# Performance work log

Measured on AMD Instinct MI355X. Metric: run time of the kernel, lower is better.

Reference implementation:

```python
import jax, jax.numpy as jnp
import numpy as np

N_U, N_V = 8192, 8192
IN_U, IN_V = 64, 64
OUT_U, OUT_V = 64, 64
RATING = 5


def setup_inputs() -> dict:
    key = jax.random.key(0)
    k1, k2, k3, k4, k5 = jax.random.split(key, 5)
    adj = jax.random.randint(k1, (N_U, N_V), 0, 6, dtype=jnp.int32)  # ratings 0..5, 0 = no edge
    u_feature = jax.random.normal(k2, (N_U, IN_U), dtype=jnp.float32)
    v_feature = jax.random.normal(k3, (N_V, IN_V), dtype=jnp.float32)
    weight_u = 0.02 * jax.random.normal(k4, (RATING, IN_V, OUT_U), dtype=jnp.float32)
    weight_v = 0.02 * jax.random.normal(k5, (RATING, IN_U, OUT_V), dtype=jnp.float32)
    return {"adj": adj, "u_feature": u_feature, "v_feature": v_feature,
            "weight_u": weight_u, "weight_v": weight_v}


def reference(adj, u_feature, v_feature, weight_u, weight_v):
    rating = weight_u.shape[0]
    dt = u_feature.dtype
    # Per-rating binary masks M_r: [R, n_u, n_v]
    ratings = jnp.arange(1, rating + 1, dtype=adj.dtype)
    masks = (adj[None, :, :] == ratings[:, None, None]).astype(dt)
    # Degree normalization (reciprocal of nonzero counts; inf -> 0)
    deg_u = jnp.sum(adj > 0, axis=1).astype(dt)  # [n_u]
    deg_v = jnp.sum(adj > 0, axis=0).astype(dt)  # [n_v]
    d_u = jnp.where(deg_u > 0, 1.0 / deg_u, 0.0)
    d_v = jnp.where(deg_v > 0, 1.0 / deg_v, 0.0)
    # Aggregate neighbor features per rating, project, sum over ratings.
    agg_u = jnp.einsum('ruv,vf->ruf', masks, v_feature)      # [R, n_u, in_v]
    out_u = jnp.einsum('ruf,rfo->uo', agg_u, weight_u)        # [n_u, out_u]
    out_u = d_u[:, None] * out_u
    agg_v = jnp.einsum('ruv,uf->rvf', masks, u_feature)      # [R, n_v, in_u]
    out_v = jnp.einsum('rvf,rfo->vo', agg_v, weight_v)        # [n_v, out_v]
    out_v = d_v[:, None] * out_v
    return (jax.nn.relu(out_u), jax.nn.relu(out_v))
```

## Files before the change

### kernel.cpp

```cpp
#include <hip/hip_runtime.h>

#define N_U 8192
#define N_V 8192
#define DIM 64
#define NR 5

typedef __attribute__((ext_vector_type(8))) short short8;
typedef __attribute__((ext_vector_type(4))) float f32x4;

__device__ inline unsigned short f2bf(float x) {
    unsigned u = __float_as_uint(x);
    return (unsigned short)((u + 0x7FFFu + ((u >> 16) & 1u)) >> 16);
}

__device__ inline size_t pfrag_idx(int r, int k, int o) {
    int ktile = k >> 5;
    int lane  = ((k >> 2) & 3) * 16 + (o & 15);
    int j     = ((k >> 4) & 1) * 4 + (k & 3);
    int n     = o >> 4;
    return ((((size_t)r * (N_V / 32) + ktile) * 4 + n) * 64 + lane) * 8 + j;
}

__global__ __launch_bounds__(256) void precompute_P(
    const float* __restrict__ u_feat, const float* __restrict__ v_feat,
    const float* __restrict__ w_u, const float* __restrict__ w_v,
    unsigned short* __restrict__ p_u, unsigned short* __restrict__ p_v)
{
    int wid  = (blockIdx.x * blockDim.x + threadIdx.x) >> 6;
    int lane = threadIdx.x & 63;
    const int tasks = 2 * NR * (N_V / 32);
    if (wid >= tasks) return;
    int dir  = wid / (NR * (N_V / 32));
    int rem  = wid % (NR * (N_V / 32));
    int r    = rem / (N_V / 32);
    int v0   = (rem % (N_V / 32)) * 32;

    const float* feat = dir ? u_feat : v_feat;
    const float* w    = dir ? w_v : w_u;
    unsigned short* dst = dir ? p_v : p_u;

    float wreg[DIM];
#pragma unroll
    for (int f = 0; f < DIM; ++f) wreg[f] = w[(r * DIM + f) * DIM + lane];

    for (int v = v0; v < v0 + 32; ++v) {
        float x = feat[(size_t)v * DIM + lane];
        float acc = 0.f;
#pragma unroll
        for (int f = 0; f < DIM; ++f) acc += __shfl(x, f) * wreg[f];
        dst[pfrag_idx(r, v, lane)] = f2bf(acc);
    }
}

template <int TRANS>
__global__ __launch_bounds__(512) void gemm_masked(
    const int* __restrict__ adj, const unsigned short* __restrict__ pfrag,
    float* __restrict__ outp, unsigned int* __restrict__ deg)
{
    __shared__ unsigned char tile[256 * 72];
    __shared__ unsigned int cnt[256];

    const int tid  = threadIdx.x;
    const int lane = tid & 63;
    const int wv   = tid >> 6;
    const int b0   = blockIdx.x * 256;
    const int k0b  = blockIdx.y * 512;

    if (tid < 256) cnt[tid] = 0;
    __syncthreads();

    f32x4 acc[2][4];
#pragma unroll
    for (int m = 0; m < 2; ++m)
#pragma unroll
        for (int n = 0; n < 4; ++n) acc[m][n] = (f32x4){0.f, 0.f, 0.f, 0.f};

    for (int kk = 0; kk < 512; kk += 64) {
        const int k0 = k0b + kk;
        if (TRANS == 0) {
#pragma unroll
            for (int it = 0; it < 8; ++it) {
                int idx4 = it * 512 + tid;
                int row  = idx4 >> 4;
                int c4   = (idx4 & 15) * 4;
                int4 a = *(const int4*)(adj + (size_t)(b0 + row) * N_V + (k0 + c4));
                unsigned packed = (a.x & 0xFF) | ((a.y & 0xFF) << 8) |
                                  ((a.z & 0xFF) << 16) | ((a.w & 0xFF) << 24);
                *(unsigned*)&tile[row * 72 + c4] = packed;
                unsigned c = (a.x != 0) + (a.y != 0) + (a.z != 0) + (a.w != 0);
                if (c) atomicAdd(&cnt[row], c);
            }
        } else {
#pragma unroll
            for (int it = 0; it < 2; ++it) {
                int bi = it * 512 + tid;
                int u4 = (bi >> 6) * 4;
                int v4 = (bi & 63) * 4;
                int4 d0 = *(const int4*)(adj + (size_t)(k0 + u4 + 0) * N_V + (b0 + v4));
                int4 d1 = *(const int4*)(adj + (size_t)(k0 + u4 + 1) * N_V + (b0 + v4));
                int4 d2 = *(const int4*)(adj + (size_t)(k0 + u4 + 2) * N_V + (b0 + v4));
                int4 d3 = *(const int4*)(adj + (size_t)(k0 + u4 + 3) * N_V + (b0 + v4));
                const int* p0 = (const int*)&d0; const int* p1 = (const int*)&d1;
                const int* p2 = (const int*)&d2; const int* p3 = (const int*)&d3;
#pragma unroll
                for (int c = 0; c < 4; ++c) {
                    int x0 = p0[c], x1 = p1[c], x2 = p2[c], x3 = p3[c];
                    unsigned packed = (x0 & 0xFF) | ((x1 & 0xFF) << 8) |
                                      ((x2 & 0xFF) << 16) | ((x3 & 0xFF) << 24);
                    *(unsigned*)&tile[(v4 + c) * 72 + u4] = packed;
                    unsigned cc = (x0 != 0) + (x1 != 0) + (x2 != 0) + (x3 != 0);
                    if (cc) atomicAdd(&cnt[v4 + c], cc);
                }
            }
        }
        __syncthreads();

#pragma unroll
        for (int k32 = 0; k32 < 64; k32 += 32) {
            const int ktile = (k0 + k32) >> 5;
            short8 amask[2][NR];
#pragma unroll
            for (int m = 0; m < 2; ++m) {
                int row  = wv * 32 + m * 16 + (lane & 15);
                int boff = row * 72 + k32 + ((lane >> 4) << 2);
                unsigned d0 = *(const unsigned*)&tile[boff];
                unsigned d1 = *(const unsigned*)&tile[boff + 16];
#pragma unroll
                for (int rr = 0; rr < NR; ++rr) {
                    short8 msk;
#pragma unroll
                    for (int j = 0; j < 4; ++j)
                        msk[j] = (short)((((d0 >> (8 * j)) & 0xFFu) == (unsigned)(rr + 1)) ? 0x3F80 : 0);
#pragma unroll
                    for (int j = 0; j < 4; ++j)
                        msk[4 + j] = (short)((((d1 >> (8 * j)) & 0xFFu) == (unsigned)(rr + 1)) ? 0x3F80 : 0);
                    amask[m][rr] = msk;
                }
            }
#pragma unroll
            for (int n = 0; n < 4; ++n) {
#pragma unroll
                for (int rr = 0; rr < NR; ++rr) {
                    const unsigned short* bp =
                        pfrag + ((((size_t)rr * (N_V / 32) + ktile) * 4 + n) * 64 + lane) * 8;
                    short8 bfrag = *(const short8*)bp;
                    acc[0][n] = __builtin_amdgcn_mfma_f32_16x16x32_bf16(amask[0][rr], bfrag, acc[0][n], 0, 0, 0);
                    acc[1][n] = __builtin_amdgcn_mfma_f32_16x16x32_bf16(amask[1][rr], bfrag, acc[1][n], 0, 0, 0);
                }
            }
        }
        __syncthreads();
    }

#pragma unroll
    for (int m = 0; m < 2; ++m) {
        int rbase = b0 + wv * 32 + m * 16 + ((lane >> 4) << 2);
#pragma unroll
        for (int n = 0; n < 4; ++n) {
#pragma unroll
            for (int q = 0; q < 4; ++q) {
                atomicAdd(&outp[(size_t)(rbase + q) * DIM + n * 16 + (lane & 15)], acc[m][n][q]);
            }
        }
    }
    if (tid < 256) atomicAdd(&deg[b0 + tid], cnt[tid]);
}

__global__ __launch_bounds__(256) void finalize_k(
    float* __restrict__ outp, const unsigned int* __restrict__ deg_u,
    const unsigned int* __restrict__ deg_v)
{
    int idx = blockIdx.x * blockDim.x + threadIdx.x;
    const int total = 2 * N_U * DIM;
    for (; idx < total; idx += gridDim.x * blockDim.x) {
        int row = idx >> 6;
        unsigned d = (row < N_U) ? deg_u[row] : deg_v[row - N_U];
        float s = d ? (1.f / (float)d) : 0.f;
        float v = outp[idx] * s;
        outp[idx] = v > 0.f ? v : 0.f;
    }
}

extern "C" void kernel_launch(void* const* d_in, const int* in_sizes, int n_in,
                              void* d_out, int out_size, void* d_ws, size_t ws_size,
                              hipStream_t stream)
{
    const int*   adj = (const int*)d_in[0];
    const float* uf  = (const float*)d_in[1];
    const float* vf  = (const float*)d_in[2];
    const float* wu  = (const float*)d_in[3];
    const float* wv  = (const float*)d_in[4];
    float* outp = (float*)d_out;

    unsigned char* ws = (unsigned char*)d_ws;
    const size_t P_BYTES = (size_t)NR * (N_V / 32) * 4 * 64 * 8 * 2;
    unsigned short* p_u  = (unsigned short*)ws;
    unsigned short* p_v  = (unsigned short*)(ws + P_BYTES);
    unsigned int*   deg_u = (unsigned int*)(ws + 2 * P_BYTES);
    unsigned int*   deg_v = (unsigned int*)(ws + 2 * P_BYTES + N_U * sizeof(unsigned int));

    hipMemsetAsync(d_out, 0, (size_t)2 * N_U * DIM * sizeof(float), stream);
    hipMemsetAsync(ws + 2 * P_BYTES, 0, (N_U + N_V) * sizeof(unsigned int), stream);

    precompute_P<<<640, 256, 0, stream>>>(uf, vf, wu, wv, p_u, p_v);

    dim3 grid(32, 16);
    gemm_masked<0><<<grid, 512, 0, stream>>>(adj, p_u, outp, deg_u);
    gemm_masked<1><<<grid, 512, 0, stream>>>(adj, p_v, outp + (size_t)N_U * DIM, deg_v);

    finalize_k<<<2048, 256, 0, stream>>>(outp, deg_u, deg_v);
}
```

Baseline: 335.0 us.

## Double-buffer adj and P tiles with async LDS loads in masked GEMM

Restructures the masked GEMM main loop into a two-stage software pipeline. P fragments are staged into shared memory with global_load_lds, and the next step's adjacency tile is prefetched into registers while MFMAs run on the current buffer. The adjacency tile shrinks to 32-wide K steps with a swizzled LDS layout to cut bank conflicts. Degree counting now uses per-thread packed register counters reduced once at the end instead of shared-memory atomics. It adds register pressure (launch bounds asks for 4 blocks) and a more complex synchronisation pattern.

```diff
diff --git a/kernel.cpp b/kernel.cpp
--- a/kernel.cpp
+++ b/kernel.cpp
@@ -4,6 +4,9 @@
 #define N_V 8192
 #define DIM 64
 #define NR 5
+#define BM 256
+#define NSTEP 16
+#define KS 32
 
 typedef __attribute__((ext_vector_type(8))) short short8;
 typedef __attribute__((ext_vector_type(4))) float f32x4;
@@ -11,6 +14,12 @@
 __device__ inline unsigned short f2bf(float x) {
     unsigned u = __float_as_uint(x);
     return (unsigned short)((u + 0x7FFFu + ((u >> 16) & 1u)) >> 16);
+}
+
+__device__ __forceinline__ void gload_lds16(const void* g, void* l) {
+    __builtin_amdgcn_global_load_lds(
+        (const __attribute__((address_space(1))) void*)g,
+        (__attribute__((address_space(3))) void*)l, 16, 0, 0);
 }
 
 __device__ inline size_t pfrag_idx(int r, int k, int o) {
@@ -53,102 +62,137 @@
 }
 
 template <int TRANS>
-__global__ __launch_bounds__(512) void gemm_masked(
+__global__ __launch_bounds__(512, 4) void gemm_masked(
     const int* __restrict__ adj, const unsigned short* __restrict__ pfrag,
     float* __restrict__ outp, unsigned int* __restrict__ deg)
 {
-    __shared__ unsigned char tile[256 * 72];
-    __shared__ unsigned int cnt[256];
+    __shared__ unsigned char  bufA[2][BM][40];
+    __shared__ unsigned short bufB[2][NR][4][64][8];
 
     const int tid  = threadIdx.x;
     const int lane = tid & 63;
     const int wv   = tid >> 6;
-    const int b0   = blockIdx.x * 256;
-    const int k0b  = blockIdx.y * 512;
-
-    if (tid < 256) cnt[tid] = 0;
+    const int b0   = blockIdx.x * BM;
+    const int kt0  = blockIdx.y * NSTEP;
+
+    f32x4 acc[2][4];
+#pragma unroll
+    for (int m = 0; m < 2; ++m)
+#pragma unroll
+        for (int n = 0; n < 4; ++n) acc[m][n] = (f32x4){0.f, 0.f, 0.f, 0.f};
+
+    unsigned cnt_pack = 0;
+    int4 pre[4];
+
+    auto issueB = [&](int s) {
+        const int p = s & 1;
+        const int kt = kt0 + s;
+        for (int c = wv; c < 20; c += 8) {
+            int rr = c >> 2, n = c & 3;
+            const unsigned short* src =
+                pfrag + ((((size_t)rr * (N_V / 32) + kt) * 4 + n) << 9) + lane * 8;
+            gload_lds16(src, (void*)&bufB[p][rr][n][0][0]);
+        }
+    };
+    auto loadAdj = [&](int s) {
+        const int kbase = (kt0 + s) * KS;
+        if (TRANS == 0) {
+#pragma unroll
+            for (int it = 0; it < 4; ++it) {
+                int idx4 = it * 512 + tid;
+                int row  = idx4 >> 3;
+                int c4   = (idx4 & 7) * 4;
+                pre[it] = *(const int4*)(adj + (size_t)(b0 + row) * N_V + (kbase + c4));
+            }
+        } else {
+            int u4 = (tid >> 6) * 4;
+            int v4 = (tid & 63) * 4;
+#pragma unroll
+            for (int c = 0; c < 4; ++c)
+                pre[c] = *(const int4*)(adj + (size_t)(kbase + u4 + c) * N_V + (b0 + v4));
+        }
+    };
+    auto packWrite = [&](int s) {
+        const int p = s & 1;
+        if (TRANS == 0) {
+#pragma unroll
+            for (int it = 0; it < 4; ++it) {
+                int idx4 = it * 512 + tid;
+                int row  = idx4 >> 3;
+                int c4   = (idx4 & 7) * 4;
+                int4 a = pre[it];
+                unsigned pk = (a.x & 0xFF) | ((a.y & 0xFF) << 8) |
+                              ((a.z & 0xFF) << 16) | ((a.w & 0xFF) << 24);
+                int w = ((c4 >> 2) + (row >> 4)) & 7;
+                *(unsigned*)&bufA[p][row][w * 4] = pk;
+                unsigned c = (a.x != 0) + (a.y != 0) + (a.z != 0) + (a.w != 0);
+                cnt_pack += c << (8 * it);
+            }
+        } else {
+            int u4 = (tid >> 6) * 4;
+            int v4 = (tid & 63) * 4;
+            const int* q0 = (const int*)&pre[0];
+            const int* q1 = (const int*)&pre[1];
+            const int* q2 = (const int*)&pre[2];
+            const int* q3 = (const int*)&pre[3];
+#pragma unroll
+            for (int cc = 0; cc < 4; ++cc) {
+                int x0 = q0[cc], x1 = q1[cc], x2 = q2[cc], x3 = q3[cc];
+                unsigned pk = (x0 & 0xFF) | ((x1 & 0xFF) << 8) |
+                              ((x2 & 0xFF) << 16) | ((x3 & 0xFF) << 24);
+                int row = v4 + cc;
+                int w = ((u4 >> 2) + (row >> 4)) & 7;
+                *(unsigned*)&bufA[p][row][w * 4] = pk;
+                unsigned c = (x0 != 0) + (x1 != 0) + (x2 != 0) + (x3 != 0);
+                cnt_pack += c << (8 * cc);
+            }
+        }
+    };
+    auto compute = [&](int s) {
+        const int p = s & 1;
+        unsigned d[2][2];
+#pragma unroll
+        for (int m = 0; m < 2; ++m) {
+            int row = wv * 32 + m * 16 + (lane & 15);
+            int sw  = (row >> 4) & 7;
+            int lg  = lane >> 4;
+            d[m][0] = *(const unsigned*)&bufA[p][row][4 * ((lg + sw) & 7)];
+            d[m][1] = *(const unsigned*)&bufA[p][row][4 * ((lg + 4 + sw) & 7)];
+        }
+        unsigned bx[2][8];
+#pragma unroll
+        for (int m = 0; m < 2; ++m)
+#pragma unroll
+            for (int j = 0; j < 4; ++j) {
+                bx[m][j]     = (d[m][0] >> (8 * j)) & 0xFFu;
+                bx[m][4 + j] = (d[m][1] >> (8 * j)) & 0xFFu;
+            }
+#pragma unroll
+        for (int rr = 0; rr < NR; ++rr) {
+            short8 am[2];
+#pragma unroll
+            for (int m = 0; m < 2; ++m)
+#pragma unroll
+                for (int j = 0; j < 8; ++j)
+                    am[m][j] = (short)(bx[m][j] == (unsigned)(rr + 1) ? 0x3F80 : 0);
+#pragma unroll
+            for (int n = 0; n < 4; ++n) {
+                short8 bf = *(const short8*)&bufB[p][rr][n][lane][0];
+                acc[0][n] = __builtin_amdgcn_mfma_f32_16x16x32_bf16(am[0], bf, acc[0][n], 0, 0, 0);
+                acc[1][n] = __builtin_amdgcn_mfma_f32_16x16x32_bf16(am[1], bf, acc[1][n], 0, 0, 0);
+            }
+        }
+    };
+
+    issueB(0);
+    loadAdj(0);
+    packWrite(0);
     __syncthreads();
 
-    f32x4 acc[2][4];
-#pragma unroll
-    for (int m = 0; m < 2; ++m)
-#pragma unroll
-        for (int n = 0; n < 4; ++n) acc[m][n] = (f32x4){0.f, 0.f, 0.f, 0.f};
-
-    for (int kk = 0; kk < 512; kk += 64) {
-        const int k0 = k0b + kk;
-        if (TRANS == 0) {
-#pragma unroll
-            for (int it = 0; it < 8; ++it) {
-                int idx4 = it * 512 + tid;
-                int row  = idx4 >> 4;
-                int c4   = (idx4 & 15) * 4;
-                int4 a = *(const int4*)(adj + (size_t)(b0 + row) * N_V + (k0 + c4));
-                unsigned packed = (a.x & 0xFF) | ((a.y & 0xFF) << 8) |
-                                  ((a.z & 0xFF) << 16) | ((a.w & 0xFF) << 24);
-                *(unsigned*)&tile[row * 72 + c4] = packed;
-                unsigned c = (a.x != 0) + (a.y != 0) + (a.z != 0) + (a.w != 0);
-                if (c) atomicAdd(&cnt[row], c);
-            }
-        } else {
-#pragma unroll
-            for (int it = 0; it < 2; ++it) {
-                int bi = it * 512 + tid;
-                int u4 = (bi >> 6) * 4;
-                int v4 = (bi & 63) * 4;
-                int4 d0 = *(const int4*)(adj + (size_t)(k0 + u4 + 0) * N_V + (b0 + v4));
-                int4 d1 = *(const int4*)(adj + (size_t)(k0 + u4 + 1) * N_V + (b0 + v4));
-                int4 d2 = *(const int4*)(adj + (size_t)(k0 + u4 + 2) * N_V + (b0 + v4));
-                int4 d3 = *(const int4*)(adj + (size_t)(k0 + u4 + 3) * N_V + (b0 + v4));
-                const int* p0 = (const int*)&d0; const int* p1 = (const int*)&d1;
-                const int* p2 = (const int*)&d2; const int* p3 = (const int*)&d3;
-#pragma unroll
-                for (int c = 0; c < 4; ++c) {
-                    int x0 = p0[c], x1 = p1[c], x2 = p2[c], x3 = p3[c];
-                    unsigned packed = (x0 & 0xFF) | ((x1 & 0xFF) << 8) |
-                                      ((x2 & 0xFF) << 16) | ((x3 & 0xFF) << 24);
-                    *(unsigned*)&tile[(v4 + c) * 72 + u4] = packed;
-                    unsigned cc = (x0 != 0) + (x1 != 0) + (x2 != 0) + (x3 != 0);
-                    if (cc) atomicAdd(&cnt[v4 + c], cc);
-                }
-            }
-        }
-        __syncthreads();
-
-#pragma unroll
-        for (int k32 = 0; k32 < 64; k32 += 32) {
-            const int ktile = (k0 + k32) >> 5;
-            short8 amask[2][NR];
-#pragma unroll
-            for (int m = 0; m < 2; ++m) {
-                int row  = wv * 32 + m * 16 + (lane & 15);
-                int boff = row * 72 + k32 + ((lane >> 4) << 2);
-                unsigned d0 = *(const unsigned*)&tile[boff];
-                unsigned d1 = *(const unsigned*)&tile[boff + 16];
-#pragma unroll
-                for (int rr = 0; rr < NR; ++rr) {
-                    short8 msk;
-#pragma unroll
-                    for (int j = 0; j < 4; ++j)
-                        msk[j] = (short)((((d0 >> (8 * j)) & 0xFFu) == (unsigned)(rr + 1)) ? 0x3F80 : 0);
-#pragma unroll
-                    for (int j = 0; j < 4; ++j)
-                        msk[4 + j] = (short)((((d1 >> (8 * j)) & 0xFFu) == (unsigned)(rr + 1)) ? 0x3F80 : 0);
-                    amask[m][rr] = msk;
-                }
-            }
-#pragma unroll
-            for (int n = 0; n < 4; ++n) {
-#pragma unroll
-                for (int rr = 0; rr < NR; ++rr) {
-                    const unsigned short* bp =
-                        pfrag + ((((size_t)rr * (N_V / 32) + ktile) * 4 + n) * 64 + lane) * 8;
-                    short8 bfrag = *(const short8*)bp;
-                    acc[0][n] = __builtin_amdgcn_mfma_f32_16x16x32_bf16(amask[0][rr], bfrag, acc[0][n], 0, 0, 0);
-                    acc[1][n] = __builtin_amdgcn_mfma_f32_16x16x32_bf16(amask[1][rr], bfrag, acc[1][n], 0, 0, 0);
-                }
-            }
-        }
+    for (int s = 0; s < NSTEP; ++s) {
+        if (s + 1 < NSTEP) { issueB(s + 1); loadAdj(s + 1); }
+        compute(s);
+        if (s + 1 < NSTEP) packWrite(s + 1);
         __syncthreads();
     }
 
@@ -156,14 +200,29 @@
     for (int m = 0; m < 2; ++m) {
         int rbase = b0 + wv * 32 + m * 16 + ((lane >> 4) << 2);
 #pragma unroll
-        for (int n = 0; n < 4; ++n) {
-#pragma unroll
-            for (int q = 0; q < 4; ++q) {
+        for (int n = 0; n < 4; ++n)
+#pragma unroll
+            for (int q = 0; q < 4; ++q)
                 atomicAdd(&outp[(size_t)(rbase + q) * DIM + n * 16 + (lane & 15)], acc[m][n][q]);
-            }
-        }
-    }
-    if (tid < 256) atomicAdd(&deg[b0 + tid], cnt[tid]);
+    }
+
+    __syncthreads();
+    unsigned* sc = (unsigned*)&bufA[0][0][0];
+    sc[tid] = cnt_pack;
+    __syncthreads();
+    if (tid < BM) {
+        unsigned tot = 0;
+        if (TRANS == 0) {
+            int it = tid >> 6, srow = tid & 63;
+#pragma unroll
+            for (int j = 0; j < 8; ++j) tot += (sc[srow * 8 + j] >> (8 * it)) & 0xFFu;
+        } else {
+            int sv = tid >> 2, cc = tid & 3;
+#pragma unroll
+            for (int j = 0; j < 8; ++j) tot += (sc[sv + 64 * j] >> (8 * cc)) & 0xFFu;
+        }
+        atomicAdd(&deg[b0 + tid], tot);
+    }
 }
 
 __global__ __launch_bounds__(256) void finalize_k(
@@ -194,8 +253,8 @@
 
     unsigned char* ws = (unsigned char*)d_ws;
     const size_t P_BYTES = (size_t)NR * (N_V / 32) * 4 * 64 * 8 * 2;
-    unsigned short* p_u  = (unsigned short*)ws;
-    unsigned short* p_v  = (unsigned short*)(ws + P_BYTES);
+    unsigned short* p_u   = (unsigned short*)ws;
+    unsigned short* p_v   = (unsigned short*)(ws + P_BYTES);
     unsigned int*   deg_u = (unsigned int*)(ws + 2 * P_BYTES);
     unsigned int*   deg_v = (unsigned int*)(ws + 2 * P_BYTES + N_U * sizeof(unsigned int));
 
@@ -204,7 +263,7 @@
 
     precompute_P<<<640, 256, 0, stream>>>(uf, vf, wu, wv, p_u, p_v);
 
-    dim3 grid(32, 16);
+    dim3 grid(N_U / BM, 16);
     gemm_masked<0><<<grid, 512, 0, stream>>>(adj, p_u, outp, deg_u);
     gemm_masked<1><<<grid, 512, 0, stream>>>(adj, p_v, outp + (size_t)N_U * DIM, deg_v);
 
```

Result: slower. 454.8 us (+35.8%).

## Stage full adjacency tile as 4-bit nibbles in LDS with prefetched loads

Applied to the files above, without the earlier changes.

Each block now loads its entire 256x512 adjacency slab into shared memory in one phase, packed as 4-bit ratings in an XOR-swizzled layout, with register double-buffered global loads. Degree counting uses wave ballots and popcount, or per-thread packed byte counters, in place of shared atomics. The compute loop then runs with no barriers, and the B-fragment layout is changed so each lane's eight k values are contiguous. This removes per-chunk syncs and LDS atomics at the cost of larger shared memory use and higher register pressure.

```diff
diff --git a/kernel.cpp b/kernel.cpp
--- a/kernel.cpp
+++ b/kernel.cpp
@@ -4,6 +4,9 @@
 #define N_V 8192
 #define DIM 64
 #define NR 5
+#define BM 256
+#define BK 512
+#define NSTEP 16
 
 typedef __attribute__((ext_vector_type(8))) short short8;
 typedef __attribute__((ext_vector_type(4))) float f32x4;
@@ -15,8 +18,9 @@
 
 __device__ inline size_t pfrag_idx(int r, int k, int o) {
     int ktile = k >> 5;
-    int lane  = ((k >> 2) & 3) * 16 + (o & 15);
-    int j     = ((k >> 4) & 1) * 4 + (k & 3);
+    int g     = (k >> 3) & 3;
+    int j     = k & 7;
+    int lane  = g * 16 + (o & 15);
     int n     = o >> 4;
     return ((((size_t)r * (N_V / 32) + ktile) * 4 + n) * 64 + lane) * 8 + j;
 }
@@ -53,20 +57,84 @@
 }
 
 template <int TRANS>
-__global__ __launch_bounds__(512) void gemm_masked(
+__global__ __launch_bounds__(512, 4) void gemm_masked(
     const int* __restrict__ adj, const unsigned short* __restrict__ pfrag,
     float* __restrict__ outp, unsigned int* __restrict__ deg)
 {
-    __shared__ unsigned char tile[256 * 72];
-    __shared__ unsigned int cnt[256];
+    __shared__ unsigned char tile[BM][256];
+    __shared__ unsigned int  cnt[BM];
 
     const int tid  = threadIdx.x;
     const int lane = tid & 63;
     const int wv   = tid >> 6;
-    const int b0   = blockIdx.x * 256;
-    const int k0b  = blockIdx.y * 512;
-
-    if (tid < 256) cnt[tid] = 0;
+    const int b0   = blockIdx.x * BM;
+    const int k0   = blockIdx.y * BK;
+
+    unsigned cpack = 0;
+
+    if (TRANS == 0) {
+        int4 pre[4], nxt[4];
+        const int sub = tid & 31;
+        auto issue = [&](int rnd, int4* dst) {
+            int row = rnd * 16 + (tid >> 5);
+            const int* base = adj + (size_t)(b0 + row) * N_V + k0 + sub * 4;
+#pragma unroll
+            for (int it = 0; it < 4; ++it) dst[it] = *(const int4*)(base + it * 128);
+        };
+        issue(0, pre);
+        for (int rnd = 0; rnd < 16; ++rnd) {
+            if (rnd + 1 < 16) issue(rnd + 1, nxt);
+            int row = rnd * 16 + (tid >> 5);
+            unsigned lo = 0, hi = 0;
+#pragma unroll
+            for (int it = 0; it < 4; ++it) {
+                int4 a = pre[it];
+                unsigned long long bx = __ballot(a.x != 0), by = __ballot(a.y != 0);
+                unsigned long long bz = __ballot(a.z != 0), bw = __ballot(a.w != 0);
+                lo += __popcll(bx & 0xFFFFFFFFull) + __popcll(by & 0xFFFFFFFFull) +
+                      __popcll(bz & 0xFFFFFFFFull) + __popcll(bw & 0xFFFFFFFFull);
+                hi += __popcll(bx >> 32) + __popcll(by >> 32) +
+                      __popcll(bz >> 32) + __popcll(bw >> 32);
+                unsigned pk = (unsigned)a.x | ((unsigned)a.y << 4) |
+                              ((unsigned)a.z << 8) | ((unsigned)a.w << 12);
+                int d  = it * 16 + (sub >> 1);
+                int dp = d ^ (row & 31);
+                *(unsigned short*)&tile[row][dp * 4 + (sub & 1) * 2] = (unsigned short)pk;
+            }
+            if ((tid & 31) == 0) cnt[row] = (lane & 32) ? hi : lo;
+#pragma unroll
+            for (int it = 0; it < 4; ++it) pre[it] = nxt[it];
+        }
+    } else {
+        const int v4 = (tid & 63) * 4;
+        int4 pre[4], nxt[4];
+        auto issue = [&](int rnd, int4* dst) {
+            int u0 = rnd * 32 + (tid >> 6) * 4;
+#pragma unroll
+            for (int c = 0; c < 4; ++c)
+                dst[c] = *(const int4*)(adj + (size_t)(k0 + u0 + c) * N_V + b0 + v4);
+        };
+        issue(0, pre);
+        for (int rnd = 0; rnd < 16; ++rnd) {
+            if (rnd + 1 < 16) issue(rnd + 1, nxt);
+            const int* q0 = (const int*)&pre[0]; const int* q1 = (const int*)&pre[1];
+            const int* q2 = (const int*)&pre[2]; const int* q3 = (const int*)&pre[3];
+            int d    = rnd * 4 + ((tid >> 6) >> 1);
+            int half = (tid >> 6) & 1;
+#pragma unroll
+            for (int cc = 0; cc < 4; ++cc) {
+                int x0 = q0[cc], x1 = q1[cc], x2 = q2[cc], x3 = q3[cc];
+                unsigned pk = (unsigned)x0 | ((unsigned)x1 << 4) |
+                              ((unsigned)x2 << 8) | ((unsigned)x3 << 12);
+                int row = v4 + cc;
+                int dp  = d ^ (row & 31);
+                *(unsigned short*)&tile[row][dp * 4 + half * 2] = (unsigned short)pk;
+                cpack += (unsigned)((x0 != 0) + (x1 != 0) + (x2 != 0) + (x3 != 0)) << (8 * cc);
+            }
+#pragma unroll
+            for (int c = 0; c < 4; ++c) pre[c] = nxt[c];
+        }
+    }
     __syncthreads();
 
     f32x4 acc[2][4];
@@ -75,95 +143,64 @@
 #pragma unroll
         for (int n = 0; n < 4; ++n) acc[m][n] = (f32x4){0.f, 0.f, 0.f, 0.f};
 
-    for (int kk = 0; kk < 512; kk += 64) {
-        const int k0 = k0b + kk;
-        if (TRANS == 0) {
-#pragma unroll
-            for (int it = 0; it < 8; ++it) {
-                int idx4 = it * 512 + tid;
-                int row  = idx4 >> 4;
-                int c4   = (idx4 & 15) * 4;
-                int4 a = *(const int4*)(adj + (size_t)(b0 + row) * N_V + (k0 + c4));
-                unsigned packed = (a.x & 0xFF) | ((a.y & 0xFF) << 8) |
-                                  ((a.z & 0xFF) << 16) | ((a.w & 0xFF) << 24);
-                *(unsigned*)&tile[row * 72 + c4] = packed;
-                unsigned c = (a.x != 0) + (a.y != 0) + (a.z != 0) + (a.w != 0);
-                if (c) atomicAdd(&cnt[row], c);
+    const int mrow = wv * 32;
+    for (int s = 0; s < NSTEP; ++s) {
+        unsigned nib[2];
+#pragma unroll
+        for (int m = 0; m < 2; ++m) {
+            int row = mrow + m * 16 + (lane & 15);
+            int d   = s * 4 + (lane >> 4);
+            nib[m] = *(const unsigned*)&tile[row][((d ^ (row & 31)) << 2)];
+        }
+        const int ktg = (k0 >> 5) + s;
+#pragma unroll
+        for (int r = 0; r < NR; ++r) {
+            short8 bf[4];
+#pragma unroll
+            for (int n = 0; n < 4; ++n)
+                bf[n] = *(const short8*)(pfrag +
+                         ((((size_t)r * (N_V / 32) + ktg) * 4 + n) * 64 + lane) * 8);
+            short8 am[2];
+#pragma unroll
+            for (int m = 0; m < 2; ++m)
+#pragma unroll
+                for (int j = 0; j < 8; ++j) {
+                    unsigned nb = (nib[m] >> (4 * j)) & 0xFu;
+                    am[m][j] = (short)(nb == (unsigned)(r + 1) ? 0x3F80 : 0);
+                }
+#pragma unroll
+            for (int n = 0; n < 4; ++n) {
+                acc[0][n] = __builtin_amdgcn_mfma_f32_16x16x32_bf16(am[0], bf[n], acc[0][n], 0, 0, 0);
+                acc[1][n] = __builtin_amdgcn_mfma_f32_16x16x32_bf16(am[1], bf[n], acc[1][n], 0, 0, 0);
             }
-        } else {
-#pragma unroll
-            for (int it = 0; it < 2; ++it) {
-                int bi = it * 512 + tid;
-                int u4 = (bi >> 6) * 4;
-                int v4 = (bi & 63) * 4;
-                int4 d0 = *(const int4*)(adj + (size_t)(k0 + u4 + 0) * N_V + (b0 + v4));
-                int4 d1 = *(const int4*)(adj + (size_t)(k0 + u4 + 1) * N_V + (b0 + v4));
-                int4 d2 = *(const int4*)(adj + (size_t)(k0 + u4 + 2) * N_V + (b0 + v4));
-                int4 d3 = *(const int4*)(adj + (size_t)(k0 + u4 + 3) * N_V + (b0 + v4));
-                const int* p0 = (const int*)&d0; const int* p1 = (const int*)&d1;
-                const int* p2 = (const int*)&d2; const int* p3 = (const int*)&d3;
-#pragma unroll
-                for (int c = 0; c < 4; ++c) {
-                    int x0 = p0[c], x1 = p1[c], x2 = p2[c], x3 = p3[c];
-                    unsigned packed = (x0 & 0xFF) | ((x1 & 0xFF) << 8) |
-                                      ((x2 & 0xFF) << 16) | ((x3 & 0xFF) << 24);
-                    *(unsigned*)&tile[(v4 + c) * 72 + u4] = packed;
-                    unsigned cc = (x0 != 0) + (x1 != 0) + (x2 != 0) + (x3 != 0);
-                    if (cc) atomicAdd(&cnt[v4 + c], cc);
-                }
-            }
-        }
+        }
+    }
+
+#pragma unroll
+    for (int m = 0; m < 2; ++m) {
+        int rbase = b0 + mrow + m * 16 + ((lane >> 4) << 2);
+#pragma unroll
+        for (int n = 0; n < 4; ++n)
+#pragma unroll
+            for (int q = 0; q < 4; ++q)
+                atomicAdd(&outp[(size_t)(rbase + q) * DIM + n * 16 + (lane & 15)], acc[m][n][q]);
+    }
+
+    if (TRANS == 0) {
+        if (tid < BM) atomicAdd(&deg[b0 + tid], cnt[tid]);
+    } else {
         __syncthreads();
-
-#pragma unroll
-        for (int k32 = 0; k32 < 64; k32 += 32) {
-            const int ktile = (k0 + k32) >> 5;
-            short8 amask[2][NR];
-#pragma unroll
-            for (int m = 0; m < 2; ++m) {
-                int row  = wv * 32 + m * 16 + (lane & 15);
-                int boff = row * 72 + k32 + ((lane >> 4) << 2);
-                unsigned d0 = *(const unsigned*)&tile[boff];
-                unsigned d1 = *(const unsigned*)&tile[boff + 16];
-#pragma unroll
-                for (int rr = 0; rr < NR; ++rr) {
-                    short8 msk;
-#pragma unroll
-                    for (int j = 0; j < 4; ++j)
-                        msk[j] = (short)((((d0 >> (8 * j)) & 0xFFu) == (unsigned)(rr + 1)) ? 0x3F80 : 0);
-#pragma unroll
-                    for (int j = 0; j < 4; ++j)
-                        msk[4 + j] = (short)((((d1 >> (8 * j)) & 0xFFu) == (unsigned)(rr + 1)) ? 0x3F80 : 0);
-                    amask[m][rr] = msk;
-                }
-            }
-#pragma unroll
-            for (int n = 0; n < 4; ++n) {
-#pragma unroll
-                for (int rr = 0; rr < NR; ++rr) {
-                    const unsigned short* bp =
-                        pfrag + ((((size_t)rr * (N_V / 32) + ktile) * 4 + n) * 64 + lane) * 8;
-                    short8 bfrag = *(const short8*)bp;
-                    acc[0][n] = __builtin_amdgcn_mfma_f32_16x16x32_bf16(amask[0][rr], bfrag, acc[0][n], 0, 0, 0);
-                    acc[1][n] = __builtin_amdgcn_mfma_f32_16x16x32_bf16(amask[1][rr], bfrag, acc[1][n], 0, 0, 0);
-                }
-            }
-        }
+        unsigned* sc = (unsigned*)&tile[0][0];
+        sc[tid] = cpack;
         __syncthreads();
-    }
-
-#pragma unroll
-    for (int m = 0; m < 2; ++m) {
-        int rbase = b0 + wv * 32 + m * 16 + ((lane >> 4) << 2);
-#pragma unroll
-        for (int n = 0; n < 4; ++n) {
-#pragma unroll
-            for (int q = 0; q < 4; ++q) {
-                atomicAdd(&outp[(size_t)(rbase + q) * DIM + n * 16 + (lane & 15)], acc[m][n][q]);
-            }
-        }
-    }
-    if (tid < 256) atomicAdd(&deg[b0 + tid], cnt[tid]);
+        if (tid < BM) {
+            unsigned tot = 0;
+            int base = tid >> 2, byte = tid & 3;
+#pragma unroll
+            for (int j = 0; j < 8; ++j) tot += (sc[j * 64 + base] >> (8 * byte)) & 0xFFu;
+            atomicAdd(&deg[b0 + tid], tot);
+        }
+    }
 }
 
 __global__ __launch_bounds__(256) void finalize_k(
@@ -194,8 +231,8 @@
 
     unsigned char* ws = (unsigned char*)d_ws;
     const size_t P_BYTES = (size_t)NR * (N_V / 32) * 4 * 64 * 8 * 2;
-    unsigned short* p_u  = (unsigned short*)ws;
-    unsigned short* p_v  = (unsigned short*)(ws + P_BYTES);
+    unsigned short* p_u   = (unsigned short*)ws;
+    unsigned short* p_v   = (unsigned short*)(ws + P_BYTES);
     unsigned int*   deg_u = (unsigned int*)(ws + 2 * P_BYTES);
     unsigned int*   deg_v = (unsigned int*)(ws + 2 * P_BYTES + N_U * sizeof(unsigned int));
 
@@ -204,7 +241,7 @@
 
     precompute_P<<<640, 256, 0, stream>>>(uf, vf, wu, wv, p_u, p_v);
 
-    dim3 grid(32, 16);
+    dim3 grid(N_U / BM, N_V / BK);
     gemm_masked<0><<<grid, 512, 0, stream>>>(adj, p_u, outp, deg_u);
     gemm_masked<1><<<grid, 512, 0, stream>>>(adj, p_v, outp + (size_t)N_U * DIM, deg_v);
 
```

After: 286.0 us. -14.6%, faster.

## Give each block full-K rows, drop LDS staging, atomics, memsets and finalize kernel

Applied to the files above, without the earlier changes.

Each 512-thread block now owns 16 output rows and walks the whole K dimension, with its 8 waves striding over k-tiles. Waves load adjacency values straight into registers in the MFMA A-fragment layout, so the LDS byte tile is gone, and they count degrees in registers. A tree reduction through shared memory combines partial sums, then wave 0 applies the degree normalisation and ReLU and writes the output directly. This removes the global atomics, both memsets and the separate finalize kernel. In exchange, the transposed direction now does strided 4-byte scalar loads, only 512 blocks run per direction, and the P fragments are no longer reused across 32-row tiles.

```diff
diff --git a/kernel.cpp b/kernel.cpp
--- a/kernel.cpp
+++ b/kernel.cpp
@@ -1,7 +1,6 @@
 #include <hip/hip_runtime.h>
 
-#define N_U 8192
-#define N_V 8192
+#define NN 8192
 #define DIM 64
 #define NR 5
 
@@ -13,12 +12,13 @@
     return (unsigned short)((u + 0x7FFFu + ((u >> 16) & 1u)) >> 16);
 }
 
-__device__ inline size_t pfrag_idx(int r, int k, int o) {
+__device__ inline int pfrag_idx(int r, int k, int o) {
     int ktile = k >> 5;
-    int lane  = ((k >> 2) & 3) * 16 + (o & 15);
-    int j     = ((k >> 4) & 1) * 4 + (k & 3);
+    int g     = (k >> 3) & 3;
+    int j     = k & 7;
+    int lane  = g * 16 + (o & 15);
     int n     = o >> 4;
-    return ((((size_t)r * (N_V / 32) + ktile) * 4 + n) * 64 + lane) * 8 + j;
+    return ((r * 256 + ktile) * 4 + n) * 512 + lane * 8 + j;
 }
 
 __global__ __launch_bounds__(256) void precompute_P(
@@ -28,12 +28,12 @@
 {
     int wid  = (blockIdx.x * blockDim.x + threadIdx.x) >> 6;
     int lane = threadIdx.x & 63;
-    const int tasks = 2 * NR * (N_V / 32);
+    const int tasks = 2 * NR * (NN / 32);
     if (wid >= tasks) return;
-    int dir  = wid / (NR * (N_V / 32));
-    int rem  = wid % (NR * (N_V / 32));
-    int r    = rem / (N_V / 32);
-    int v0   = (rem % (N_V / 32)) * 32;
+    int dir  = wid / (NR * (NN / 32));
+    int rem  = wid % (NR * (NN / 32));
+    int r    = rem / (NN / 32);
+    int v0   = (rem % (NN / 32)) * 32;
 
     const float* feat = dir ? u_feat : v_feat;
     const float* w    = dir ? w_v : w_u;
@@ -52,132 +52,118 @@
     }
 }
 
-template <int TRANS>
-__global__ __launch_bounds__(512) void gemm_masked(
+template <int DIR>
+__global__ __launch_bounds__(512, 4) void gemm_dir(
     const int* __restrict__ adj, const unsigned short* __restrict__ pfrag,
-    float* __restrict__ outp, unsigned int* __restrict__ deg)
+    float* __restrict__ outp)
 {
-    __shared__ unsigned char tile[256 * 72];
-    __shared__ unsigned int cnt[256];
+    __shared__ float redf[4][16][66];
+    __shared__ int   redd[8][16];
 
     const int tid  = threadIdx.x;
     const int lane = tid & 63;
     const int wv   = tid >> 6;
-    const int b0   = blockIdx.x * 256;
-    const int k0b  = blockIdx.y * 512;
+    const int row  = lane & 15;
+    const int g    = lane >> 4;
+    const int b0   = blockIdx.x * 16;
 
-    if (tid < 256) cnt[tid] = 0;
-    __syncthreads();
+    f32x4 acc[4];
+#pragma unroll
+    for (int n = 0; n < 4; ++n) acc[n] = (f32x4){0.f, 0.f, 0.f, 0.f};
+    int dcnt = 0;
 
-    f32x4 acc[2][4];
+#pragma unroll 2
+    for (int kt = wv; kt < NN / 32; kt += 8) {
+        int a[8];
+        if (DIR == 0) {
+            const int* ap = adj + (b0 + row) * NN + kt * 32 + g * 8;
+            int4 x = *(const int4*)ap;
+            int4 y = *(const int4*)(ap + 4);
+            a[0] = x.x; a[1] = x.y; a[2] = x.z; a[3] = x.w;
+            a[4] = y.x; a[5] = y.y; a[6] = y.z; a[7] = y.w;
+        } else {
+            const int* ap = adj + (kt * 32 + g * 8) * NN + b0 + row;
 #pragma unroll
-    for (int m = 0; m < 2; ++m)
+            for (int j = 0; j < 8; ++j) a[j] = ap[j * NN];
+        }
 #pragma unroll
-        for (int n = 0; n < 4; ++n) acc[m][n] = (f32x4){0.f, 0.f, 0.f, 0.f};
+        for (int j = 0; j < 8; ++j) dcnt += (a[j] != 0);
 
-    for (int kk = 0; kk < 512; kk += 64) {
-        const int k0 = k0b + kk;
-        if (TRANS == 0) {
+        const int kb = kt << 11;
 #pragma unroll
-            for (int it = 0; it < 8; ++it) {
-                int idx4 = it * 512 + tid;
-                int row  = idx4 >> 4;
-                int c4   = (idx4 & 15) * 4;
-                int4 a = *(const int4*)(adj + (size_t)(b0 + row) * N_V + (k0 + c4));
-                unsigned packed = (a.x & 0xFF) | ((a.y & 0xFF) << 8) |
-                                  ((a.z & 0xFF) << 16) | ((a.w & 0xFF) << 24);
-                *(unsigned*)&tile[row * 72 + c4] = packed;
-                unsigned c = (a.x != 0) + (a.y != 0) + (a.z != 0) + (a.w != 0);
-                if (c) atomicAdd(&cnt[row], c);
-            }
-        } else {
+        for (int r = 0; r < NR; ++r) {
+            short8 am;
 #pragma unroll
-            for (int it = 0; it < 2; ++it) {
-                int bi = it * 512 + tid;
-                int u4 = (bi >> 6) * 4;
-                int v4 = (bi & 63) * 4;
-                int4 d0 = *(const int4*)(adj + (size_t)(k0 + u4 + 0) * N_V + (b0 + v4));
-                int4 d1 = *(const int4*)(adj + (size_t)(k0 + u4 + 1) * N_V + (b0 + v4));
-                int4 d2 = *(const int4*)(adj + (size_t)(k0 + u4 + 2) * N_V + (b0 + v4));
-                int4 d3 = *(const int4*)(adj + (size_t)(k0 + u4 + 3) * N_V + (b0 + v4));
-                const int* p0 = (const int*)&d0; const int* p1 = (const int*)&d1;
-                const int* p2 = (const int*)&d2; const int* p3 = (const int*)&d3;
-#pragma unroll
-                for (int c = 0; c < 4; ++c) {
-                    int x0 = p0[c], x1 = p1[c], x2 = p2[c], x3 = p3[c];
-                    unsigned packed = (x0 & 0xFF) | ((x1 & 0xFF) << 8) |
-                                      ((x2 & 0xFF) << 16) | ((x3 & 0xFF) << 24);
-                    *(unsigned*)&tile[(v4 + c) * 72 + u4] = packed;
-                    unsigned cc = (x0 != 0) + (x1 != 0) + (x2 != 0) + (x3 != 0);
-                    if (cc) atomicAdd(&cnt[v4 + c], cc);
-                }
-            }
-        }
-        __syncthreads();
-
-#pragma unroll
-        for (int k32 = 0; k32 < 64; k32 += 32) {
-            const int ktile = (k0 + k32) >> 5;
-            short8 amask[2][NR];
-#pragma unroll
-            for (int m = 0; m < 2; ++m) {
-                int row  = wv * 32 + m * 16 + (lane & 15);
-                int boff = row * 72 + k32 + ((lane >> 4) << 2);
-                unsigned d0 = *(const unsigned*)&tile[boff];
-                unsigned d1 = *(const unsigned*)&tile[boff + 16];
-#pragma unroll
-                for (int rr = 0; rr < NR; ++rr) {
-                    short8 msk;
-#pragma unroll
-                    for (int j = 0; j < 4; ++j)
-                        msk[j] = (short)((((d0 >> (8 * j)) & 0xFFu) == (unsigned)(rr + 1)) ? 0x3F80 : 0);
-#pragma unroll
-                    for (int j = 0; j < 4; ++j)
-                        msk[4 + j] = (short)((((d1 >> (8 * j)) & 0xFFu) == (unsigned)(rr + 1)) ? 0x3F80 : 0);
-                    amask[m][rr] = msk;
-                }
-            }
+            for (int j = 0; j < 8; ++j)
+                am[j] = (short)(a[j] == r + 1 ? 0x3F80 : 0);
+            const unsigned short* pb = pfrag + r * (256 * 2048) + kb + (lane << 3);
 #pragma unroll
             for (int n = 0; n < 4; ++n) {
-#pragma unroll
-                for (int rr = 0; rr < NR; ++rr) {
-                    const unsigned short* bp =
-                        pfrag + ((((size_t)rr * (N_V / 32) + ktile) * 4 + n) * 64 + lane) * 8;
-                    short8 bfrag = *(const short8*)bp;
-                    acc[0][n] = __builtin_amdgcn_mfma_f32_16x16x32_bf16(amask[0][rr], bfrag, acc[0][n], 0, 0, 0);
-                    acc[1][n] = __builtin_amdgcn_mfma_f32_16x16x32_bf16(amask[1][rr], bfrag, acc[1][n], 0, 0, 0);
-                }
-            }
-        }
-        __syncthreads();
-    }
-
-#pragma unroll
-    for (int m = 0; m < 2; ++m) {
-        int rbase = b0 + wv * 32 + m * 16 + ((lane >> 4) << 2);
-#pragma unroll
-        for (int n = 0; n < 4; ++n) {
-#pragma unroll
-            for (int q = 0; q < 4; ++q) {
-                atomicAdd(&outp[(size_t)(rbase + q) * DIM + n * 16 + (lane & 15)], acc[m][n][q]);
+                short8 bf = *(const short8*)(pb + (n << 9));
+                acc[n] = __builtin_amdgcn_mfma_f32_16x16x32_bf16(am, bf, acc[n], 0, 0, 0);
             }
         }
     }
-    if (tid < 256) atomicAdd(&deg[b0 + tid], cnt[tid]);
-}
 
-__global__ __launch_bounds__(256) void finalize_k(
-    float* __restrict__ outp, const unsigned int* __restrict__ deg_u,
-    const unsigned int* __restrict__ deg_v)
-{
-    int idx = blockIdx.x * blockDim.x + threadIdx.x;
-    const int total = 2 * N_U * DIM;
-    for (; idx < total; idx += gridDim.x * blockDim.x) {
-        int row = idx >> 6;
-        unsigned d = (row < N_U) ? deg_u[row] : deg_v[row - N_U];
-        float s = d ? (1.f / (float)d) : 0.f;
-        float v = outp[idx] * s;
-        outp[idx] = v > 0.f ? v : 0.f;
+    dcnt += __shfl_xor(dcnt, 16);
+    dcnt += __shfl_xor(dcnt, 32);
+    if (lane < 16) redd[wv][lane] = dcnt;
+
+    if (wv >= 4) {
+#pragma unroll
+        for (int n = 0; n < 4; ++n)
+#pragma unroll
+            for (int q = 0; q < 4; ++q)
+                redf[wv - 4][g * 4 + q][n * 16 + row] = acc[n][q];
+    }
+    __syncthreads();
+    if (wv < 4) {
+#pragma unroll
+        for (int n = 0; n < 4; ++n)
+#pragma unroll
+            for (int q = 0; q < 4; ++q)
+                acc[n][q] += redf[wv][g * 4 + q][n * 16 + row];
+    }
+    __syncthreads();
+    if (wv == 2 || wv == 3) {
+#pragma unroll
+        for (int n = 0; n < 4; ++n)
+#pragma unroll
+            for (int q = 0; q < 4; ++q)
+                redf[wv - 2][g * 4 + q][n * 16 + row] = acc[n][q];
+    }
+    __syncthreads();
+    if (wv < 2) {
+#pragma unroll
+        for (int n = 0; n < 4; ++n)
+#pragma unroll
+            for (int q = 0; q < 4; ++q)
+                acc[n][q] += redf[wv][g * 4 + q][n * 16 + row];
+    }
+    __syncthreads();
+    if (wv == 1) {
+#pragma unroll
+        for (int n = 0; n < 4; ++n)
+#pragma unroll
+            for (int q = 0; q < 4; ++q)
+                redf[0][g * 4 + q][n * 16 + row] = acc[n][q];
+    }
+    __syncthreads();
+
+    if (wv == 0) {
+#pragma unroll
+        for (int q = 0; q < 4; ++q) {
+            int r4 = g * 4 + q;
+            int dsum = 0;
+#pragma unroll
+            for (int w = 0; w < 8; ++w) dsum += redd[w][r4];
+            float s = dsum ? 1.f / (float)dsum : 0.f;
+#pragma unroll
+            for (int n = 0; n < 4; ++n) {
+                float v = (acc[n][q] + redf[0][r4][n * 16 + row]) * s;
+                outp[(b0 + r4) * DIM + n * 16 + row] = v > 0.f ? v : 0.f;
+            }
+        }
     }
 }
 
@@ -193,20 +179,12 @@
     float* outp = (float*)d_out;
 
     unsigned char* ws = (unsigned char*)d_ws;
-    const size_t P_BYTES = (size_t)NR * (N_V / 32) * 4 * 64 * 8 * 2;
-    unsigned short* p_u  = (unsigned short*)ws;
-    unsigned short* p_v  = (unsigned short*)(ws + P_BYTES);
-    unsigned int*   deg_u = (unsigned int*)(ws + 2 * P_BYTES);
-    unsigned int*   deg_v = (unsigned int*)(ws + 2 * P_BYTES + N_U * sizeof(unsigned int));
-
-    hipMemsetAsync(d_out, 0, (size_t)2 * N_U * DIM * sizeof(float), stream);
-    hipMemsetAsync(ws + 2 * P_BYTES, 0, (N_U + N_V) * sizeof(unsigned int), stream);
+    const size_t P_BYTES = (size_t)NR * (NN / 32) * 4 * 64 * 8 * 2;
+    unsigned short* p_u = (unsigned short*)ws;
+    unsigned short* p_v = (unsigned short*)(ws + P_BYTES);
 
     precompute_P<<<640, 256, 0, stream>>>(uf, vf, wu, wv, p_u, p_v);
 
-    dim3 grid(32, 16);
-    gemm_masked<0><<<grid, 512, 0, stream>>>(adj, p_u, outp, deg_u);
-    gemm_masked<1><<<grid, 512, 0, stream>>>(adj, p_v, outp + (size_t)N_U * DIM, deg_v);
-
-    finalize_k<<<2048, 256, 0, stream>>>(outp, deg_u, deg_v);
+    gemm_dir<0><<<NN / 16, 512, 0, stream>>>(adj, p_u, outp);
+    gemm_dir<1><<<NN / 16, 512, 0, stream>>>(adj, p_v, outp + (size_t)NN * DIM);
 }
```

Result: slower. 390.4 us (+16.5%).
